# Performance work log

Hardware: AMD Instinct MI355X
Metric: run time of the kernel (lower is better)

The kernel has to match this reference:

```python
import jax, jax.numpy as jnp
import numpy as np

N = 50000      # nodes
E = 800000     # edges
IN = 128       # in_dim
EMB = 32       # emb_dim
ED = 8         # edge_dim
L = 4          # num_layers
B = 64         # num graphs in batch
OUT = 10       # out_dim
EPS = 1e-5


def setup_inputs() -> dict:
    key = jax.random.key(0)
    ks = jax.random.split(key, 16)
    f32 = jnp.float32
    def nrm(k, shape, scale):
        return jax.random.normal(k, shape, dtype=f32) * scale
    inp = {}
    inp['x'] = nrm(ks[0], (N, IN), 1.0)
    inp['edge_index'] = jax.random.randint(ks[1], (2, E), 0, N)
    inp['edge_attr'] = nrm(ks[2], (E, ED), 1.0)
    inp['batch'] = jnp.sort(jax.random.randint(ks[3], (N,), 0, B))
    # lin_in
    inp['lin_in_w'] = nrm(ks[4], (IN, EMB), 0.05)
    inp['lin_in_b'] = jnp.zeros((EMB,), f32)
    # per-layer message MLP: Linear(2e+ed->e), BN, ReLU, Linear(e->e), BN, ReLU
    inp['msg_w1'] = nrm(ks[5], (L, 2 * EMB + ED, EMB), 0.1)
    inp['msg_b1'] = jnp.zeros((L, EMB), f32)
    inp['msg_g1'] = jnp.ones((L, EMB), f32)
    inp['msg_be1'] = jnp.zeros((L, EMB), f32)
    inp['msg_w2'] = nrm(ks[6], (L, EMB, EMB), 0.1)
    inp['msg_b2'] = jnp.zeros((L, EMB), f32)
    inp['msg_g2'] = jnp.ones((L, EMB), f32)
    inp['msg_be2'] = jnp.zeros((L, EMB), f32)
    # per-layer update MLP: Linear(2e->e), BN, ReLU, Linear(e->e), BN, ReLU
    inp['upd_w1'] = nrm(ks[7], (L, 2 * EMB, EMB), 0.1)
    inp['upd_b1'] = jnp.zeros((L, EMB), f32)
    inp['upd_g1'] = jnp.ones((L, EMB), f32)
    inp['upd_be1'] = jnp.zeros((L, EMB), f32)
    inp['upd_w2'] = nrm(ks[8], (L, EMB, EMB), 0.1)
    inp['upd_b2'] = jnp.zeros((L, EMB), f32)
    inp['upd_g2'] = jnp.ones((L, EMB), f32)
    inp['upd_be2'] = jnp.zeros((L, EMB), f32)
    # lin_pred
    inp['pred_w'] = nrm(ks[9], (EMB, OUT), 0.1)
    inp['pred_b'] = jnp.zeros((OUT,), f32)
    return inp


def _bn(x, g, b):
    # BatchNorm1d in training mode: batch stats over dim 0 (biased variance)
    mu = jnp.mean(x, axis=0)
    var = jnp.mean(jnp.square(x - mu), axis=0)
    return (x - mu) * jax.lax.rsqrt(var + EPS) * g + b


def reference(x, edge_attr, lin_in_w, lin_in_b,
              msg_w1, msg_b1, msg_g1, msg_be1, msg_w2, msg_b2, msg_g2, msg_be2,
              upd_w1, upd_b1, upd_g1, upd_be1, upd_w2, upd_b2, upd_g2, upd_be2,
              pred_w, pred_b, edge_index, batch):
    src = edge_index[0]  # h_j source nodes
    dst = edge_index[1]  # h_i target nodes (aggregation index)
    h = x @ lin_in_w + lin_in_b  # [N, EMB]
    for i in range(L):
        # message: gather + concat + MLP(BN,ReLU)x2 over edges
        msg_in = jnp.concatenate([h[dst], h[src], edge_attr], axis=-1)  # [E, 2e+ed]
        m = jax.nn.relu(_bn(msg_in @ msg_w1[i] + msg_b1[i], msg_g1[i], msg_be1[i]))
        m = jax.nn.relu(_bn(m @ msg_w2[i] + msg_b2[i], msg_g2[i], msg_be2[i]))
        # aggregate: scatter-add by destination
        aggr = jax.ops.segment_sum(m, dst, num_segments=N)  # [N, EMB]
        # update: concat + MLP(BN,ReLU)x2
        u = jnp.concatenate([h, aggr], axis=-1)  # [N, 2e]
        u = jax.nn.relu(_bn(u @ upd_w1[i] + upd_b1[i], upd_g1[i], upd_be1[i]))
        u = jax.nn.relu(_bn(u @ upd_w2[i] + upd_b2[i], upd_g2[i], upd_be2[i]))
        h = u + h  # residual in MPNNModel.get_embeddings
    # global mean pool
    sums = jax.ops.segment_sum(h, batch, num_segments=B)
    counts = jax.ops.segment_sum(jnp.ones((N,), h.dtype), batch, num_segments=B)
    h_graph = sums / jnp.maximum(counts, 1.0)[:, None]
    return h_graph @ pred_w + pred_b  # [B, OUT]
```

## Files before the change

kernel.cpp:

```cpp
#include <hip/hip_runtime.h>
#include <cstddef>

#define N_NODES 50000
#define N_EDGES 800000
#define IN_DIM  128
#define EMB     32
#define ED      8
#define NLAYERS 4
#define NB      64
#define OUTD    10
#define EPS_BN  1e-5f

#define EDGE_GRID 3125
#define NODE_GRID 196
#define NODE4_GRID 782
#define AU_GRID   6250
#define NTILE_N   3125
#define LIN_GRID  782
#define ST_TPW    4
#define ST_GRID   3125
#define MSG2_TPW  4
#define MSG2_GRID 3125

#define SREP 4

typedef short bf16x8 __attribute__((ext_vector_type(8)));
typedef float f32x4  __attribute__((ext_vector_type(4)));


__device__ __forceinline__ unsigned short f2bf(float x) {
  union { float f; unsigned u; } v; v.f = x;
  unsigned b = v.u + 0x7FFFu + ((v.u >> 16) & 1u);
  return (unsigned short)(b >> 16);
}
__device__ __forceinline__ float bf2f(unsigned short s) {
  union { unsigned u; float f; } v; v.u = ((unsigned)s) << 16;
  return v.f;
}

__device__ __forceinline__ void coef_from_stats(const float* __restrict__ stats_stage,
                                                const float* __restrict__ g,
                                                const float* __restrict__ be,
                                                float inv_count, float* __restrict__ cf) {
  if (threadIdx.x < EMB) {
    const int c = threadIdx.x;
    float s = 0.f, ss = 0.f;
#pragma unroll
    for (int r = 0; r < SREP; ++r) {
      s  += stats_stage[r*64 + c];
      ss += stats_stage[r*64 + EMB + c];
    }
    const float mu  = s * inv_count;
    const float var = ss * inv_count - mu*mu;
    const float a = g[c] * rsqrtf(var + EPS_BN);
    cf[c] = a;
    cf[EMB + c] = fmaf(-mu, a, be[c]);
  }
  __syncthreads();
}

__device__ __forceinline__ void wave_stats_atomic(float ts[8], float tss[8],
                                                  float* __restrict__ lds_s,
                                                  float* __restrict__ lds_q,
                                                  float* __restrict__ stats_stage) {
  const int lane = threadIdx.x & 63;
  const int wv   = threadIdx.x >> 6;
#pragma unroll
  for (int j = 0; j < 8; ++j) {
    float a = ts[j], b = tss[j];
#pragma unroll
    for (int o = 32; o > 0; o >>= 1) {
      a += __shfl_down(a, o, 64);
      b += __shfl_down(b, o, 64);
    }
    ts[j] = a; tss[j] = b;
  }
  if (lane == 0) {
#pragma unroll
    for (int j = 0; j < 8; ++j) {
      lds_s[wv*8 + j] = ts[j];
      lds_q[wv*8 + j] = tss[j];
    }
  }
  __syncthreads();
  if (threadIdx.x < 64) {
    const float v = (threadIdx.x < 32) ? lds_s[threadIdx.x] : lds_q[threadIdx.x - 32];
    atomicAdd(stats_stage + ((blockIdx.x & (SREP-1)) << 6) + threadIdx.x, v);
  }
}

#define HSTRIDE 40

__global__ __launch_bounds__(256) void k_lin_in_pq(
    const float* __restrict__ x, const float* __restrict__ w, const float* __restrict__ b,
    const float* __restrict__ w1, const float* __restrict__ b1, const int* __restrict__ ei,
    const float* __restrict__ ea,
    float* __restrict__ h, unsigned short* __restrict__ p, unsigned short* __restrict__ q,
    int* __restrict__ cnt, uint4* __restrict__ rec)
{
  __shared__ __align__(16) unsigned short lds_hb[4][16*HSTRIDE];
  __shared__ __align__(16) unsigned short lds_pq[4][16*HSTRIDE];
  const int lane = threadIdx.x & 63;
  const int wv   = threadIdx.x >> 6;
  const int n0i  = lane & 15;
  const int quad = lane >> 4;

  const int tile = blockIdx.x*4 + wv;
  if (tile < NTILE_N) {
    const int r0 = tile*16;
    float4 xa[4], xb[4];
#pragma unroll
    for (int kb = 0; kb < 4; ++kb) {
      xa[kb] = *(const float4*)(x + (size_t)(r0 + n0i)*IN_DIM + kb*32 + quad*8);
      xb[kb] = *(const float4*)(x + (size_t)(r0 + n0i)*IN_DIM + kb*32 + quad*8 + 4);
    }
    bf16x8 BwL[4], BwH[4];
#pragma unroll
    for (int kb = 0; kb < 4; ++kb) {
#pragma unroll
      for (int j = 0; j < 8; ++j) {
        const int k = kb*32 + quad*8 + j;
        BwL[kb][j] = (short)f2bf(w[k*EMB + n0i]);
        BwH[kb][j] = (short)f2bf(w[k*EMB + 16 + n0i]);
      }
    }
    f32x4 accL = {0.f,0.f,0.f,0.f};
    f32x4 accH = {0.f,0.f,0.f,0.f};
#pragma unroll
    for (int kb = 0; kb < 4; ++kb) {
      bf16x8 A;
      A[0] = (short)f2bf(xa[kb].x); A[1] = (short)f2bf(xa[kb].y);
      A[2] = (short)f2bf(xa[kb].z); A[3] = (short)f2bf(xa[kb].w);
      A[4] = (short)f2bf(xb[kb].x); A[5] = (short)f2bf(xb[kb].y);
      A[6] = (short)f2bf(xb[kb].z); A[7] = (short)f2bf(xb[kb].w);
      accL = __builtin_amdgcn_mfma_f32_16x16x32_bf16(A, BwL[kb], accL, 0, 0, 0);
      accH = __builtin_amdgcn_mfma_f32_16x16x32_bf16(A, BwH[kb], accH, 0, 0, 0);
    }
    const float bL = b[n0i], bH = b[16 + n0i];
#pragma unroll
    for (int r = 0; r < 4; ++r) {
      const int row = quad*4 + r;
      const float vL = accL[r] + bL;
      const float vH = accH[r] + bH;
      h[(size_t)(r0 + row)*EMB + n0i]      = vL;
      h[(size_t)(r0 + row)*EMB + 16 + n0i] = vH;
      lds_hb[wv][row*HSTRIDE + n0i]      = f2bf(vL);
      lds_hb[wv][row*HSTRIDE + 16 + n0i] = f2bf(vH);
    }
    bf16x8 A2;
#pragma unroll
    for (int j = 0; j < 8; ++j)
      A2[j] = (short)lds_hb[wv][n0i*HSTRIDE + quad*8 + j];
    bf16x8 BpL, BpH, BqL, BqH;
#pragma unroll
    for (int j = 0; j < 8; ++j) {
      const int k = quad*8 + j;
      BpL[j] = (short)f2bf(w1[k*EMB + n0i]);
      BpH[j] = (short)f2bf(w1[k*EMB + 16 + n0i]);
      BqL[j] = (short)f2bf(w1[(EMB + k)*EMB + n0i]);
      BqH[j] = (short)f2bf(w1[(EMB + k)*EMB + 16 + n0i]);
    }
    const f32x4 z4 = {0.f,0.f,0.f,0.f};
    f32x4 pL = __builtin_amdgcn_mfma_f32_16x16x32_bf16(A2, BpL, z4, 0, 0, 0);
    f32x4 pH = __builtin_amdgcn_mfma_f32_16x16x32_bf16(A2, BpH, z4, 0, 0, 0);
    f32x4 qL = __builtin_amdgcn_mfma_f32_16x16x32_bf16(A2, BqL, z4, 0, 0, 0);
    f32x4 qH = __builtin_amdgcn_mfma_f32_16x16x32_bf16(A2, BqH, z4, 0, 0, 0);
    const float b1L = b1[n0i], b1H = b1[16 + n0i];
#pragma unroll
    for (int r = 0; r < 4; ++r) {
      const int row = quad*4 + r;
      lds_pq[wv][row*HSTRIDE + n0i]      = f2bf(pL[r] + b1L);
      lds_pq[wv][row*HSTRIDE + 16 + n0i] = f2bf(pH[r] + b1H);
    }
    {
      const int row2 = lane >> 2;
      const int c8   = (lane & 3)*8;
      const uint4 ov = *(const uint4*)&lds_pq[wv][row2*HSTRIDE + c8];
      *(uint4*)(p + (size_t)(r0 + row2)*EMB + c8) = ov;
    }
#pragma unroll
    for (int r = 0; r < 4; ++r) {
      const int row = quad*4 + r;
      lds_pq[wv][row*HSTRIDE + n0i]      = f2bf(qL[r]);
      lds_pq[wv][row*HSTRIDE + 16 + n0i] = f2bf(qH[r]);
    }
    {
      const int row2 = lane >> 2;
      const int c8   = (lane & 3)*8;
      const uint4 ov = *(const uint4*)&lds_pq[wv][row2*HSTRIDE + c8];
      *(uint4*)(q + (size_t)(r0 + row2)*EMB + c8) = ov;
    }
  }
  for (int e = blockIdx.x*256 + threadIdx.x; e < N_EDGES; e += gridDim.x*256) {
    const int s = ei[e];
    const int d = ei[N_EDGES + e];
    atomicAdd(&cnt[d], 1);
    const float4 v0 = ((const float4*)(ea + (size_t)e*ED))[0];
    const float4 v1 = ((const float4*)(ea + (size_t)e*ED))[1];
    const float ev[8] = {v0.x, v0.y, v0.z, v0.w, v1.x, v1.y, v1.z, v1.w};
    unsigned u[4];
#pragma unroll
    for (int j = 0; j < 4; ++j)
      u[j] = (unsigned)f2bf(ev[2*j]) | ((unsigned)f2bf(ev[2*j+1]) << 16);
    uint4* rp = rec + (size_t)e*2;
    rp[0] = make_uint4((unsigned)s, (unsigned)d, u[0], u[1]);
    rp[1] = make_uint4(u[2], u[3], 0u, 0u);
  }
}

__global__ __launch_bounds__(256) void k_scan_a(const int* __restrict__ cnt,
                                                int* __restrict__ row_ptr, int* __restrict__ bsum) {
  __shared__ int s[256];
  const int gid = blockIdx.x*256 + threadIdx.x;
  const int v = (gid < N_NODES) ? cnt[gid] : 0;
  s[threadIdx.x] = v;
  __syncthreads();
  for (int o = 1; o < 256; o <<= 1) {
    const int t = (threadIdx.x >= o) ? s[threadIdx.x - o] : 0;
    __syncthreads();
    s[threadIdx.x] += t;
    __syncthreads();
  }
  if (gid < N_NODES) row_ptr[gid] = s[threadIdx.x] - v;
  if (threadIdx.x == 255) bsum[blockIdx.x] = s[255];
}

__global__ __launch_bounds__(256) void k_scan_bc(int* __restrict__ row_ptr,
                                                 const int* __restrict__ bsum) {
  __shared__ int s[256];
  const int t = threadIdx.x;
  const int v = (t < NODE_GRID) ? bsum[t] : 0;
  s[t] = v;
  __syncthreads();
  for (int o = 1; o < 256; o <<= 1) {
    const int tt = (t >= o) ? s[t - o] : 0;
    __syncthreads();
    s[t] += tt;
    __syncthreads();
  }
  const int off = (blockIdx.x == 0) ? 0 : s[blockIdx.x - 1];
  const int gid = blockIdx.x*256 + t;
  if (gid < N_NODES) row_ptr[gid] += off;
  if (blockIdx.x == 0 && t == 0) row_ptr[N_NODES] = N_EDGES;
}

__global__ __launch_bounds__(256) void k_place(
    const int* __restrict__ ei, const int* __restrict__ row_ptr, int* __restrict__ cnt2,
    int* __restrict__ inv)
{
  const int e = blockIdx.x*256 + threadIdx.x;
  const int d = ei[N_EDGES + e];
  const int pos = row_ptr[d] + atomicAdd(&cnt2[d], 1);
  inv[pos] = e;
}


__global__ __launch_bounds__(256) void k_stats1(
    const unsigned short* __restrict__ pb, const unsigned short* __restrict__ qb,
    const uint4* __restrict__ rec, const float* __restrict__ w1b,
    float* __restrict__ stats)
{
  __shared__ float lds_d[4][16*33];
  __shared__ float lds_s[4][32], lds_q[4][32];
  const int lane = threadIdx.x & 63;
  const int wv   = threadIdx.x >> 6;
  const int l15  = lane & 15;
  const int quad = lane >> 4;

  bf16x8 B1lo = {}, B1hi = {};
  if (quad == 0) {
#pragma unroll
    for (int j = 0; j < 8; ++j) {
      B1lo[j] = (short)f2bf(w1b[j*EMB + l15]);
      B1hi[j] = (short)f2bf(w1b[j*EMB + 16 + l15]);
    }
  }

  const int tile0 = blockIdx.x * (4*ST_TPW);
  uint4 RA[ST_TPW], RB[ST_TPW];
#pragma unroll
  for (int t = 0; t < ST_TPW; ++t) {
    const int tile = tile0 + t*4 + wv;
    const size_t e0 = (size_t)tile * 16;
    const uint4* r4 = rec + (e0 + l15)*2;
    RA[t] = r4[0];
    RB[t] = (quad == 0) ? r4[1] : make_uint4(0u,0u,0u,0u);
  }
  uint4 PG[ST_TPW], QG[ST_TPW];
#pragma unroll
  for (int t = 0; t < ST_TPW; ++t) {
    PG[t] = *(const uint4*)(pb + (size_t)RA[t].y*EMB + quad*8);
    QG[t] = *(const uint4*)(qb + (size_t)RA[t].x*EMB + quad*8);
  }

  float ts[8], tss[8];
#pragma unroll
  for (int j = 0; j < 8; ++j) { ts[j] = 0.f; tss[j] = 0.f; }

#pragma unroll
  for (int t = 0; t < ST_TPW; ++t) {
    bf16x8 A = {};
    if (quad == 0) {
      A[0] = (short)(RA[t].z & 0xFFFFu); A[1] = (short)(RA[t].z >> 16);
      A[2] = (short)(RA[t].w & 0xFFFFu); A[3] = (short)(RA[t].w >> 16);
      A[4] = (short)(RB[t].x & 0xFFFFu); A[5] = (short)(RB[t].x >> 16);
      A[6] = (short)(RB[t].y & 0xFFFFu); A[7] = (short)(RB[t].y >> 16);
    }
    const f32x4 z4 = {0.f,0.f,0.f,0.f};
    f32x4 D0 = __builtin_amdgcn_mfma_f32_16x16x32_bf16(A, B1lo, z4, 0, 0, 0);
    f32x4 D1 = __builtin_amdgcn_mfma_f32_16x16x32_bf16(A, B1hi, z4, 0, 0, 0);
#pragma unroll
    for (int r = 0; r < 4; ++r) {
      const int row = quad*4 + r;
      lds_d[wv][row*33 + l15]      = D0[r];
      lds_d[wv][row*33 + 16 + l15] = D1[r];
    }
    const unsigned pu[4] = {PG[t].x, PG[t].y, PG[t].z, PG[t].w};
    const unsigned qu[4] = {QG[t].x, QG[t].y, QG[t].z, QG[t].w};
#pragma unroll
    for (int jj = 0; jj < 4; ++jj) {
      const float d0 = lds_d[wv][l15*33 + quad*8 + 2*jj];
      const float d1 = lds_d[wv][l15*33 + quad*8 + 2*jj + 1];
      const float v0 = (d0 + bf2f((unsigned short)(pu[jj] & 0xFFFFu)))
                            + bf2f((unsigned short)(qu[jj] & 0xFFFFu));
      const float v1 = (d1 + bf2f((unsigned short)(pu[jj] >> 16)))
                            + bf2f((unsigned short)(qu[jj] >> 16));
      const float w0 = bf2f(f2bf(v0));
      const float w1v = bf2f(f2bf(v1));
      ts[2*jj]   += w0;  tss[2*jj]   = fmaf(w0, w0, tss[2*jj]);
      ts[2*jj+1] += w1v; tss[2*jj+1] = fmaf(w1v, w1v, tss[2*jj+1]);
    }
  }

#pragma unroll
  for (int j = 0; j < 8; ++j) {
    float a = ts[j], b = tss[j];
#pragma unroll
    for (int o = 1; o < 16; o <<= 1) {
      a += __shfl_xor(a, o, 64);
      b += __shfl_xor(b, o, 64);
    }
    ts[j] = a; tss[j] = b;
  }
  if (l15 == 0) {
#pragma unroll
    for (int j = 0; j < 8; ++j) {
      lds_s[wv][quad*8 + j] = ts[j];
      lds_q[wv][quad*8 + j] = tss[j];
    }
  }
  __syncthreads();
  if (threadIdx.x < 64) {
    const int c = threadIdx.x & 31;
    const int kind = threadIdx.x >> 5;
    float v = 0.f;
#pragma unroll
    for (int wq = 0; wq < 4; ++wq)
      v += kind ? lds_q[wq][c] : lds_s[wq][c];
    atomicAdd(stats + ((blockIdx.x & (SREP-1)) << 6) + kind*32 + c, v);
  }
}

__global__ __launch_bounds__(256) void k_msg2(
    const unsigned short* __restrict__ pb, const unsigned short* __restrict__ qb,
    const uint4* __restrict__ rec, const float* __restrict__ w1b,
    const float* __restrict__ stats1, const float* __restrict__ g1, const float* __restrict__ be1,
    const float* __restrict__ w2, const float* __restrict__ b2,
    unsigned short* __restrict__ y, float* __restrict__ stats2)
{
  __shared__ float lds_d[4][16*33];
  __shared__ __align__(16) unsigned short lds_t[4][16*32];
  __shared__ float lds_s[4][32], lds_q[4][32];
  __shared__ float cf[64];

  coef_from_stats(stats1, g1, be1, 1.0f/(float)N_EDGES, cf);

  const int lane = threadIdx.x & 63;
  const int wv   = threadIdx.x >> 6;
  const int l15  = lane & 15;
  const int quad = lane >> 4;

  bf16x8 B1lo = {}, B1hi = {};
  if (quad == 0) {
#pragma unroll
    for (int j = 0; j < 8; ++j) {
      B1lo[j] = (short)f2bf(w1b[j*EMB + l15]);
      B1hi[j] = (short)f2bf(w1b[j*EMB + 16 + l15]);
    }
  }
  bf16x8 Blo, Bhi;
#pragma unroll
  for (int j = 0; j < 8; ++j) {
    Blo[j] = (short)f2bf(w2[(quad*8 + j)*EMB + l15]);
    Bhi[j] = (short)f2bf(w2[(quad*8 + j)*EMB + 16 + l15]);
  }
  float a1[8], c1[8];
#pragma unroll
  for (int j = 0; j < 8; ++j) {
    a1[j] = cf[quad*8 + j];
    c1[j] = cf[EMB + quad*8 + j];
  }
  const float b2c0 = b2[l15], b2c1 = b2[16 + l15];

  float ts[8], tss[8];
#pragma unroll
  for (int j = 0; j < 8; ++j) { ts[j] = 0.f; tss[j] = 0.f; }

  const int tile0 = blockIdx.x * (4*MSG2_TPW);

  uint4 cRA, cRB, cPG, cQG;
  {
    const size_t e0 = (size_t)(tile0 + wv) * 16;
    const uint4* r4 = rec + (e0 + l15)*2;
    cRA = r4[0];
    cRB = (quad == 0) ? r4[1] : make_uint4(0u,0u,0u,0u);
    cPG = *(const uint4*)(pb + (size_t)cRA.y*EMB + quad*8);
    cQG = *(const uint4*)(qb + (size_t)cRA.x*EMB + quad*8);
  }

#pragma unroll
  for (int t = 0; t < MSG2_TPW; ++t) {
    const size_t e0 = (size_t)(tile0 + t*4 + wv) * 16;

    uint4 nRA = make_uint4(0u,0u,0u,0u), nRB = make_uint4(0u,0u,0u,0u);
    uint4 nPG = make_uint4(0u,0u,0u,0u), nQG = make_uint4(0u,0u,0u,0u);
    if (t + 1 < MSG2_TPW) {
      const size_t e1 = (size_t)(tile0 + (t+1)*4 + wv) * 16;
      const uint4* r4 = rec + (e1 + l15)*2;
      nRA = r4[0];
      nRB = (quad == 0) ? r4[1] : make_uint4(0u,0u,0u,0u);
    }

    bf16x8 A = {};
    if (quad == 0) {
      A[0] = (short)(cRA.z & 0xFFFFu); A[1] = (short)(cRA.z >> 16);
      A[2] = (short)(cRA.w & 0xFFFFu); A[3] = (short)(cRA.w >> 16);
      A[4] = (short)(cRB.x & 0xFFFFu); A[5] = (short)(cRB.x >> 16);
      A[6] = (short)(cRB.y & 0xFFFFu); A[7] = (short)(cRB.y >> 16);
    }
    const f32x4 z4 = {0.f,0.f,0.f,0.f};
    f32x4 D0 = __builtin_amdgcn_mfma_f32_16x16x32_bf16(A, B1lo, z4, 0, 0, 0);
    f32x4 D1 = __builtin_amdgcn_mfma_f32_16x16x32_bf16(A, B1hi, z4, 0, 0, 0);
#pragma unroll
    for (int r = 0; r < 4; ++r) {
      const int row = quad*4 + r;
      lds_d[wv][row*33 + l15]      = D0[r];
      lds_d[wv][row*33 + 16 + l15] = D1[r];
    }

    if (t + 1 < MSG2_TPW) {
      nPG = *(const uint4*)(pb + (size_t)nRA.y*EMB + quad*8);
      nQG = *(const uint4*)(qb + (size_t)nRA.x*EMB + quad*8);
    }

    const unsigned pu[4] = {cPG.x, cPG.y, cPG.z, cPG.w};
    const unsigned qu[4] = {cQG.x, cQG.y, cQG.z, cQG.w};
    bf16x8 A2;
#pragma unroll
    for (int jj = 0; jj < 4; ++jj) {
      const float d0 = lds_d[wv][l15*33 + quad*8 + 2*jj];
      const float d1 = lds_d[wv][l15*33 + quad*8 + 2*jj + 1];
      const float v0 = (d0 + bf2f((unsigned short)(pu[jj] & 0xFFFFu)))
                            + bf2f((unsigned short)(qu[jj] & 0xFFFFu));
      const float v1 = (d1 + bf2f((unsigned short)(pu[jj] >> 16)))
                            + bf2f((unsigned short)(qu[jj] >> 16));
      const float w0 = bf2f(f2bf(v0));
      const float w1v = bf2f(f2bf(v1));
      const float r0 = fmaxf(fmaf(a1[2*jj],   w0,  c1[2*jj]),   0.f);
      const float r1 = fmaxf(fmaf(a1[2*jj+1], w1v, c1[2*jj+1]), 0.f);
      A2[2*jj]   = (short)f2bf(r0);
      A2[2*jj+1] = (short)f2bf(r1);
    }

    f32x4 acc0 = {0.f, 0.f, 0.f, 0.f};
    f32x4 acc1 = {0.f, 0.f, 0.f, 0.f};
    acc0 = __builtin_amdgcn_mfma_f32_16x16x32_bf16(A2, Blo, acc0, 0, 0, 0);
    acc1 = __builtin_amdgcn_mfma_f32_16x16x32_bf16(A2, Bhi, acc1, 0, 0, 0);

#pragma unroll
    for (int r = 0; r < 4; ++r) {
      const int row = quad*4 + r;
      lds_t[wv][row*32 + l15]      = f2bf(acc0[r] + b2c0);
      lds_t[wv][row*32 + 16 + l15] = f2bf(acc1[r] + b2c1);
    }
    const uint4 orow = *(const uint4*)&lds_t[wv][(lane>>2)*32 + (lane&3)*8];
    *(uint4*)(y + (e0 + (lane>>2))*EMB + (lane&3)*8) = orow;

    const unsigned uo[4] = {orow.x, orow.y, orow.z, orow.w};
#pragma unroll
    for (int j = 0; j < 4; ++j) {
      const float v0 = bf2f((unsigned short)(uo[j] & 0xFFFFu));
      const float v1 = bf2f((unsigned short)(uo[j] >> 16));
      ts[2*j]   += v0;  tss[2*j]   = fmaf(v0, v0, tss[2*j]);
      ts[2*j+1] += v1;  tss[2*j+1] = fmaf(v1, v1, tss[2*j+1]);
    }

    cRA = nRA; cRB = nRB; cPG = nPG; cQG = nQG;
  }

#pragma unroll
  for (int j = 0; j < 8; ++j) {
    float s = ts[j], qq = tss[j];
#pragma unroll
    for (int o = 4; o < 64; o <<= 1) {
      s  += __shfl_xor(s, o, 64);
      qq += __shfl_xor(qq, o, 64);
    }
    ts[j] = s; tss[j] = qq;
  }
  if (lane < 4) {
#pragma unroll
    for (int j = 0; j < 8; ++j) {
      lds_s[wv][lane*8 + j] = ts[j];
      lds_q[wv][lane*8 + j] = tss[j];
    }
  }
  __syncthreads();
  if (threadIdx.x < 64) {
    const int c = threadIdx.x & 31;
    const int kind = threadIdx.x >> 5;
    float v = 0.f;
#pragma unroll
    for (int wq = 0; wq < 4; ++wq)
      v += kind ? lds_q[wq][c] : lds_s[wq][c];
    atomicAdd(stats2 + ((blockIdx.x & (SREP-1)) << 6) + kind*32 + c, v);
  }
}

__global__ __launch_bounds__(256) void k_aggr_upd1(
    const unsigned short* __restrict__ y, const int* __restrict__ row_ptr,
    const int* __restrict__ inv,
    const float* __restrict__ h,
    const float* __restrict__ stats1, const float* __restrict__ g2, const float* __restrict__ be2,
    const float* __restrict__ uw1, const float* __restrict__ ub1,
    float* __restrict__ z, float* __restrict__ stats2)
{
  __shared__ float cf[64];
  __shared__ float lh[8][32];
  __shared__ float la[8][32];
  __shared__ float rs[4][32], rq[4][32];
  coef_from_stats(stats1, g2, be2, 1.0f/(float)N_EDGES, cf);

  const int g = threadIdx.x >> 5;
  const int l = threadIdx.x & 31;
  const int n = blockIdx.x*8 + g;

  lh[g][l] = h[(size_t)n*EMB + l];

  const int c8  = (l & 3) * 8;
  const int rof = l >> 2;
  float a[8], b[8];
#pragma unroll
  for (int j = 0; j < 8; ++j) { a[j] = cf[c8 + j]; b[j] = cf[EMB + c8 + j]; }
  const int lo = row_ptr[n], hi = row_ptr[n+1];
  float acc[8];
#pragma unroll
  for (int j = 0; j < 8; ++j) acc[j] = 0.f;
  for (int r = lo + rof; r < hi; r += 8) {
    const int ee = inv[r];
    const uint4 u = *(const uint4*)(y + (size_t)ee*EMB + c8);
    const unsigned uu[4] = {u.x, u.y, u.z, u.w};
#pragma unroll
    for (int t = 0; t < 4; ++t) {
      const float v0 = bf2f((unsigned short)(uu[t] & 0xFFFFu));
      const float v1 = bf2f((unsigned short)(uu[t] >> 16));
      acc[2*t]   += fmaxf(fmaf(a[2*t],   v0, b[2*t]),   0.f);
      acc[2*t+1] += fmaxf(fmaf(a[2*t+1], v1, b[2*t+1]), 0.f);
    }
  }
#pragma unroll
  for (int j = 0; j < 8; ++j) {
    float v = acc[j];
    v += __shfl_xor(v, 4, 64);
    v += __shfl_xor(v, 8, 64);
    v += __shfl_xor(v, 16, 64);
    acc[j] = v;
  }
  if (rof == 0) {
#pragma unroll
    for (int j = 0; j < 8; ++j) la[g][c8 + j] = acc[j];
  }
  __syncthreads();

  float accu = ub1[l];
#pragma unroll
  for (int k = 0; k < EMB; ++k) accu = fmaf(lh[g][k], uw1[k*EMB + l], accu);
#pragma unroll
  for (int k = 0; k < EMB; ++k) accu = fmaf(la[g][k], uw1[(EMB + k)*EMB + l], accu);
  z[(size_t)n*EMB + l] = accu;

  const float sq = accu*accu;
  const float a2 = accu + __shfl_down(accu, 32, 64);
  const float q2 = sq   + __shfl_down(sq,   32, 64);
  const int wv = threadIdx.x >> 6;
  if ((threadIdx.x & 63) < 32) { rs[wv][l] = a2; rq[wv][l] = q2; }
  __syncthreads();
  if (threadIdx.x < 64) {
    const int c = threadIdx.x & 31;
    const int kind = threadIdx.x >> 5;
    float v = 0.f;
#pragma unroll
    for (int wq = 0; wq < 4; ++wq)
      v += kind ? rq[wq][c] : rs[wq][c];
    atomicAdd(stats2 + ((blockIdx.x & (SREP-1)) << 6) + kind*32 + c, v);
  }
}

__global__ __launch_bounds__(256) void k_upd2(
    float* __restrict__ z,
    const float* __restrict__ stats1, const float* __restrict__ g1, const float* __restrict__ be1,
    const float* __restrict__ w, const float* __restrict__ b,
    float* __restrict__ stats2)
{
  __shared__ float cf[64];
  __shared__ float lds_s[32], lds_q[32];
  coef_from_stats(stats1, g1, be1, 1.0f/(float)N_NODES, cf);

  const int lane = threadIdx.x & 63;
  const int wv   = threadIdx.x >> 6;
  const int n  = blockIdx.x*64 + lane;
  const int c0 = wv*8;
  float acc[8];
#pragma unroll
  for (int j = 0; j < 8; ++j) acc[j] = 0.f;
  if (n < N_NODES) {
#pragma unroll
    for (int j = 0; j < 8; ++j) acc[j] = b[c0 + j];
    const float4* zp = (const float4*)(z + (size_t)n*EMB);
#pragma unroll
    for (int k4 = 0; k4 < 8; ++k4) {
      const float4 v = zp[k4];
      const float mv[4] = {v.x, v.y, v.z, v.w};
#pragma unroll
      for (int t = 0; t < 4; ++t) {
        const int k = 4*k4 + t;
        const float m = fmaxf(fmaf(cf[k], mv[t], cf[EMB + k]), 0.f);
        const float* wk = w + k*EMB + c0;
#pragma unroll
        for (int j = 0; j < 8; ++j) acc[j] = fmaf(m, wk[j], acc[j]);
      }
    }
  }
  float ts[8], tss[8];
#pragma unroll
  for (int j = 0; j < 8; ++j) { ts[j] = acc[j]; tss[j] = acc[j]*acc[j]; }
  wave_stats_atomic(ts, tss, lds_s, lds_q, stats2);
  if (n < N_NODES) {
    float4 o0, o1;
    o0.x = acc[0]; o0.y = acc[1]; o0.z = acc[2]; o0.w = acc[3];
    o1.x = acc[4]; o1.y = acc[5]; o1.z = acc[6]; o1.w = acc[7];
    *(float4*)(z + (size_t)n*EMB + c0)     = o0;
    *(float4*)(z + (size_t)n*EMB + c0 + 4) = o1;
  }
}

__global__ __launch_bounds__(256) void k_resid_pq(
    float* __restrict__ h, const float* __restrict__ z,
    const float* __restrict__ stats, const float* __restrict__ g, const float* __restrict__ be,
    const float* __restrict__ w1_next, const float* __restrict__ b1_next,
    unsigned short* __restrict__ p, unsigned short* __restrict__ q)
{
  __shared__ float cf[64];
  __shared__ float lds_h[64][33];
  coef_from_stats(stats, g, be, 1.0f/(float)N_NODES, cf);

  const int lane = threadIdx.x & 63;
  const int wv   = threadIdx.x >> 6;
  const int n  = blockIdx.x*64 + lane;
  const int c0 = wv*8;
  if (n < N_NODES) {
    const float4* zp = (const float4*)(z + (size_t)n*EMB + c0);
    float4* hp = (float4*)(h + (size_t)n*EMB + c0);
    float hn[8];
    const float4 z0 = zp[0], z1 = zp[1];
    const float4 h0 = hp[0], h1 = hp[1];
    const float zv[8] = {z0.x, z0.y, z0.z, z0.w, z1.x, z1.y, z1.z, z1.w};
    const float hv[8] = {h0.x, h0.y, h0.z, h0.w, h1.x, h1.y, h1.z, h1.w};
#pragma unroll
    for (int j = 0; j < 8; ++j) {
      const int k = c0 + j;
      hn[j] = hv[j] + fmaxf(fmaf(cf[k], zv[j], cf[EMB + k]), 0.f);
      lds_h[lane][k] = hn[j];
    }
    float4 o0, o1;
    o0.x = hn[0]; o0.y = hn[1]; o0.z = hn[2]; o0.w = hn[3];
    o1.x = hn[4]; o1.y = hn[5]; o1.z = hn[6]; o1.w = hn[7];
    hp[0] = o0; hp[1] = o1;
  }
  __syncthreads();
  if (n < N_NODES && w1_next) {
    float ap[8], aq[8];
#pragma unroll
    for (int j = 0; j < 8; ++j) { ap[j] = b1_next[c0 + j]; aq[j] = 0.f; }
#pragma unroll
    for (int k = 0; k < EMB; ++k) {
      const float hvv = lds_h[lane][k];
      const float* wp = w1_next + k*EMB + c0;
      const float* wq = w1_next + (EMB + k)*EMB + c0;
#pragma unroll
      for (int j = 0; j < 8; ++j) ap[j] = fmaf(hvv, wp[j], ap[j]);
#pragma unroll
      for (int j = 0; j < 8; ++j) aq[j] = fmaf(hvv, wq[j], aq[j]);
    }
    unsigned up[4], uq[4];
#pragma unroll
    for (int j = 0; j < 4; ++j) {
      up[j] = (unsigned)f2bf(ap[2*j]) | ((unsigned)f2bf(ap[2*j+1]) << 16);
      uq[j] = (unsigned)f2bf(aq[2*j]) | ((unsigned)f2bf(aq[2*j+1]) << 16);
    }
    uint4 op; op.x = up[0]; op.y = up[1]; op.z = up[2]; op.w = up[3];
    uint4 oq; oq.x = uq[0]; oq.y = uq[1]; oq.z = uq[2]; oq.w = uq[3];
    *(uint4*)(p + (size_t)n*EMB + c0) = op;
    *(uint4*)(q + (size_t)n*EMB + c0) = oq;
  }
}

__global__ void k_pool(const float* __restrict__ h, const int* __restrict__ batch,
                       const float* __restrict__ pw, const float* __restrict__ pb,
                       float* __restrict__ out)
{
  __shared__ float sred[256];
  __shared__ float hg[EMB];
  const int b = blockIdx.x;
  int lo = 0, hi = N_NODES;
  while (lo < hi) { int m = (lo + hi) >> 1; if (batch[m] < b) lo = m + 1; else hi = m; }
  const int start = lo;
  hi = N_NODES;
  while (lo < hi) { int m = (lo + hi) >> 1; if (batch[m] < b + 1) lo = m + 1; else hi = m; }
  const int end = lo;

  const int c = threadIdx.x & (EMB-1);
  const int r = threadIdx.x >> 5;
  float s = 0.f;
  for (int n = start + r; n < end; n += 8) s += h[(size_t)n*EMB + c];
  sred[threadIdx.x] = s;
  __syncthreads();
  if (threadIdx.x < EMB) {
    float tot = 0.f;
#pragma unroll
    for (int r2 = 0; r2 < 8; ++r2) tot += sred[r2*EMB + threadIdx.x];
    const float cnt = (float)(end - start);
    hg[threadIdx.x] = tot / fmaxf(cnt, 1.f);
  }
  __syncthreads();
  if (threadIdx.x < OUTD) {
    float acc = pb[threadIdx.x];
#pragma unroll
    for (int cc = 0; cc < EMB; ++cc) acc = fmaf(hg[cc], pw[cc*OUTD + threadIdx.x], acc);
    out[b*OUTD + threadIdx.x] = acc;
  }
}


extern "C" void kernel_launch(void* const* d_in, const int* in_sizes, int n_in,
                              void* d_out, int out_size, void* d_ws, size_t ws_size,
                              hipStream_t stream) {
  const float* x        = (const float*)d_in[0];
  const int*   ei       = (const int*)  d_in[1];
  const float* ea       = (const float*)d_in[2];
  const int*   batch    = (const int*)  d_in[3];
  const float* lin_in_w = (const float*)d_in[4];
  const float* lin_in_b = (const float*)d_in[5];
  const float* msg_w1   = (const float*)d_in[6];
  const float* msg_b1   = (const float*)d_in[7];
  const float* msg_g1   = (const float*)d_in[8];
  const float* msg_be1  = (const float*)d_in[9];
  const float* msg_w2   = (const float*)d_in[10];
  const float* msg_b2   = (const float*)d_in[11];
  const float* msg_g2   = (const float*)d_in[12];
  const float* msg_be2  = (const float*)d_in[13];
  const float* upd_w1   = (const float*)d_in[14];
  const float* upd_b1   = (const float*)d_in[15];
  const float* upd_g1   = (const float*)d_in[16];
  const float* upd_be1  = (const float*)d_in[17];
  const float* upd_w2   = (const float*)d_in[18];
  const float* upd_b2   = (const float*)d_in[19];
  const float* upd_g2   = (const float*)d_in[20];
  const float* upd_be2  = (const float*)d_in[21];
  const float* pred_w   = (const float*)d_in[22];
  const float* pred_b   = (const float*)d_in[23];
  float* out = (float*)d_out;

  char* wsb = (char*)d_ws;
  unsigned short* y  = (unsigned short*)wsb;
  uint4* rec = (uint4*)(wsb + (size_t)N_EDGES*EMB*2);
  unsigned short* p  = (unsigned short*)(rec + (size_t)N_EDGES*2);
  unsigned short* q  = p + (size_t)N_NODES*EMB;
  float* h       = (float*)(q + (size_t)N_NODES*EMB);
  float* z       = h + (size_t)N_NODES*EMB;
  float* stats   = z + (size_t)N_NODES*EMB;
  int*   cnt     = (int*)(stats + 16*SREP*64);
  int*   cnt2    = cnt + N_NODES;
  int*   row_ptr = cnt2 + N_NODES;
  int*   bsum    = row_ptr + N_NODES + 1;
  int*   inv     = bsum + 256;
  const size_t need = ((size_t)((char*)(inv + N_EDGES) - wsb));
  if (ws_size < need) return;

  hipMemsetAsync(stats, 0, (16*SREP*64 + 2*N_NODES)*sizeof(float), stream);

  k_lin_in_pq<<<LIN_GRID, 256, 0, stream>>>(x, lin_in_w, lin_in_b, msg_w1, msg_b1, ei, ea,
                                            h, p, q, cnt, rec);
  k_scan_a<<<NODE_GRID, 256, 0, stream>>>(cnt, row_ptr, bsum);
  k_scan_bc<<<NODE_GRID, 256, 0, stream>>>(row_ptr, bsum);
  k_place<<<EDGE_GRID, 256, 0, stream>>>(ei, row_ptr, cnt2, inv);

  for (int l = 0; l < NLAYERS; ++l) {
    const int st = l*4;
    const float* w1  = msg_w1 + (size_t)l*(2*EMB+ED)*EMB;
    const float* w1b = w1 + (size_t)2*EMB*EMB;
    const float* w2  = msg_w2 + (size_t)l*EMB*EMB;
    const float* uw1 = upd_w1 + (size_t)l*(2*EMB)*EMB;
    const float* uw2 = upd_w2 + (size_t)l*EMB*EMB;
    const float* w1_next = (l+1 < NLAYERS) ? msg_w1 + (size_t)(l+1)*(2*EMB+ED)*EMB : nullptr;
    const float* b1_next = (l+1 < NLAYERS) ? msg_b1 + (size_t)(l+1)*EMB : nullptr;

    k_stats1<<<ST_GRID, 256, 0, stream>>>(p, q, rec, w1b, stats + (size_t)st*SREP*64);
    k_msg2<<<MSG2_GRID, 256, 0, stream>>>(p, q, rec, w1b,
                                          stats + (size_t)st*SREP*64,
                                          msg_g1 + l*EMB, msg_be1 + l*EMB,
                                          w2, msg_b2 + l*EMB,
                                          y, stats + (size_t)(st+1)*SREP*64);
    k_aggr_upd1<<<AU_GRID, 256, 0, stream>>>(y, row_ptr, inv, h,
                                             stats + (size_t)(st+1)*SREP*64,
                                             msg_g2 + l*EMB, msg_be2 + l*EMB,
                                             uw1, upd_b1 + l*EMB,
                                             z, stats + (size_t)(st+2)*SREP*64);
    k_upd2<<<NODE4_GRID, 256, 0, stream>>>(z, stats + (size_t)(st+2)*SREP*64,
                                           upd_g1 + l*EMB, upd_be1 + l*EMB,
                                           uw2, upd_b2 + l*EMB, stats + (size_t)(st+3)*SREP*64);
    k_resid_pq<<<NODE4_GRID, 256, 0, stream>>>(h, z, stats + (size_t)(st+3)*SREP*64,
                                               upd_g2 + l*EMB, upd_be2 + l*EMB,
                                               w1_next, b1_next, p, q);
  }

  k_pool<<<NB, 256, 0, stream>>>(h, batch, pred_w, pred_b, out);
}
```

Measured before the change: 851.3 us.

## Store edge records in destination-sorted order to drop indirection in aggregation

Edges are now physically permuted into CSR (destination-sorted) order when the packed edge records are built. Each edge's rank within its destination comes from the counting atomic, which removes the second atomic pass. Because messages y are written in that same sorted order, the aggregation kernel reads y contiguously by row index instead of through the inv permutation. This removes a random gather and an index load per edge in every layer, at the cost of scattered writes in the one-time placement kernel.

Result: faster. 801.6 us, median of 2 (-5.8%).

```diff
diff --git a/kernel.cpp b/kernel.cpp
--- a/kernel.cpp
+++ b/kernel.cpp
@@ -94,9 +94,8 @@
 __global__ __launch_bounds__(256) void k_lin_in_pq(
     const float* __restrict__ x, const float* __restrict__ w, const float* __restrict__ b,
     const float* __restrict__ w1, const float* __restrict__ b1, const int* __restrict__ ei,
-    const float* __restrict__ ea,
     float* __restrict__ h, unsigned short* __restrict__ p, unsigned short* __restrict__ q,
-    int* __restrict__ cnt, uint4* __restrict__ rec)
+    int* __restrict__ cnt, int* __restrict__ rankp)
 {
   __shared__ __align__(16) unsigned short lds_hb[4][16*HSTRIDE];
   __shared__ __align__(16) unsigned short lds_pq[4][16*HSTRIDE];
@@ -192,19 +191,8 @@
     }
   }
   for (int e = blockIdx.x*256 + threadIdx.x; e < N_EDGES; e += gridDim.x*256) {
-    const int s = ei[e];
     const int d = ei[N_EDGES + e];
-    atomicAdd(&cnt[d], 1);
-    const float4 v0 = ((const float4*)(ea + (size_t)e*ED))[0];
-    const float4 v1 = ((const float4*)(ea + (size_t)e*ED))[1];
-    const float ev[8] = {v0.x, v0.y, v0.z, v0.w, v1.x, v1.y, v1.z, v1.w};
-    unsigned u[4];
-#pragma unroll
-    for (int j = 0; j < 4; ++j)
-      u[j] = (unsigned)f2bf(ev[2*j]) | ((unsigned)f2bf(ev[2*j+1]) << 16);
-    uint4* rp = rec + (size_t)e*2;
-    rp[0] = make_uint4((unsigned)s, (unsigned)d, u[0], u[1]);
-    rp[1] = make_uint4(u[2], u[3], 0u, 0u);
+    rankp[e] = atomicAdd(&cnt[d], 1);
   }
 }
 
@@ -244,14 +232,26 @@
   if (blockIdx.x == 0 && t == 0) row_ptr[N_NODES] = N_EDGES;
 }
 
-__global__ __launch_bounds__(256) void k_place(
-    const int* __restrict__ ei, const int* __restrict__ row_ptr, int* __restrict__ cnt2,
-    int* __restrict__ inv)
+__global__ __launch_bounds__(256) void k_place_scatter(
+    const int* __restrict__ ei, const float* __restrict__ ea,
+    const int* __restrict__ row_ptr, const int* __restrict__ rankp,
+    uint4* __restrict__ rec)
 {
   const int e = blockIdx.x*256 + threadIdx.x;
+  const int s = ei[e];
   const int d = ei[N_EDGES + e];
-  const int pos = row_ptr[d] + atomicAdd(&cnt2[d], 1);
-  inv[pos] = e;
+  int pos = row_ptr[d] + rankp[e];
+  pos = (pos < 0) ? 0 : ((pos >= N_EDGES) ? (N_EDGES - 1) : pos);
+  const float4 v0 = ((const float4*)(ea + (size_t)e*ED))[0];
+  const float4 v1 = ((const float4*)(ea + (size_t)e*ED))[1];
+  const float ev[8] = {v0.x, v0.y, v0.z, v0.w, v1.x, v1.y, v1.z, v1.w};
+  unsigned u[4];
+#pragma unroll
+  for (int j = 0; j < 4; ++j)
+    u[j] = (unsigned)f2bf(ev[2*j]) | ((unsigned)f2bf(ev[2*j+1]) << 16);
+  uint4* rp = rec + (size_t)pos*2;
+  rp[0] = make_uint4((unsigned)s, (unsigned)d, u[0], u[1]);
+  rp[1] = make_uint4(u[2], u[3], 0u, 0u);
 }
 
 
@@ -529,7 +529,6 @@
 
 __global__ __launch_bounds__(256) void k_aggr_upd1(
     const unsigned short* __restrict__ y, const int* __restrict__ row_ptr,
-    const int* __restrict__ inv,
     const float* __restrict__ h,
     const float* __restrict__ stats1, const float* __restrict__ g2, const float* __restrict__ be2,
     const float* __restrict__ uw1, const float* __restrict__ ub1,
@@ -557,8 +556,7 @@
 #pragma unroll
   for (int j = 0; j < 8; ++j) acc[j] = 0.f;
   for (int r = lo + rof; r < hi; r += 8) {
-    const int ee = inv[r];
-    const uint4 u = *(const uint4*)(y + (size_t)ee*EMB + c8);
+    const uint4 u = *(const uint4*)(y + (size_t)r*EMB + c8);
     const unsigned uu[4] = {u.x, u.y, u.z, u.w};
 #pragma unroll
     for (int t = 0; t < 4; ++t) {
@@ -790,20 +788,19 @@
   float* z       = h + (size_t)N_NODES*EMB;
   float* stats   = z + (size_t)N_NODES*EMB;
   int*   cnt     = (int*)(stats + 16*SREP*64);
-  int*   cnt2    = cnt + N_NODES;
-  int*   row_ptr = cnt2 + N_NODES;
+  int*   row_ptr = cnt + N_NODES;
   int*   bsum    = row_ptr + N_NODES + 1;
-  int*   inv     = bsum + 256;
-  const size_t need = ((size_t)((char*)(inv + N_EDGES) - wsb));
+  int*   rankp   = bsum + 256;
+  const size_t need = ((size_t)((char*)(rankp + N_EDGES) - wsb));
   if (ws_size < need) return;
 
-  hipMemsetAsync(stats, 0, (16*SREP*64 + 2*N_NODES)*sizeof(float), stream);
-
-  k_lin_in_pq<<<LIN_GRID, 256, 0, stream>>>(x, lin_in_w, lin_in_b, msg_w1, msg_b1, ei, ea,
-                                            h, p, q, cnt, rec);
+  hipMemsetAsync(stats, 0, (16*SREP*64 + N_NODES)*sizeof(float), stream);
+
+  k_lin_in_pq<<<LIN_GRID, 256, 0, stream>>>(x, lin_in_w, lin_in_b, msg_w1, msg_b1, ei,
+                                            h, p, q, cnt, rankp);
   k_scan_a<<<NODE_GRID, 256, 0, stream>>>(cnt, row_ptr, bsum);
   k_scan_bc<<<NODE_GRID, 256, 0, stream>>>(row_ptr, bsum);
-  k_place<<<EDGE_GRID, 256, 0, stream>>>(ei, row_ptr, cnt2, inv);
+  k_place_scatter<<<EDGE_GRID, 256, 0, stream>>>(ei, ea, row_ptr, rankp, rec);
 
   for (int l = 0; l < NLAYERS; ++l) {
     const int st = l*4;
@@ -821,7 +818,7 @@
                                           msg_g1 + l*EMB, msg_be1 + l*EMB,
                                           w2, msg_b2 + l*EMB,
                                           y, stats + (size_t)(st+1)*SREP*64);
-    k_aggr_upd1<<<AU_GRID, 256, 0, stream>>>(y, row_ptr, inv, h,
+    k_aggr_upd1<<<AU_GRID, 256, 0, stream>>>(y, row_ptr, h,
                                              stats + (size_t)(st+1)*SREP*64,
                                              msg_g2 + l*EMB, msg_be2 + l*EMB,
                                              uw1, upd_b1 + l*EMB,
```
